# Kernel tuning notes

Measured on AMD Instinct MI355X. Metric: run time of the kernel, lower is better.

Reference implementation:

```python
import jax, jax.numpy as jnp
import numpy as np

D_MODEL = 1024
N_HEADS = 16
HEAD_DIM = D_MODEL // N_HEADS  # 64
BATCH, SEQ = 2, 2048
MASK_FILL = -1000000000.0


def setup_inputs() -> dict:
    key = jax.random.key(0)
    ks = jax.random.split(key, 13)
    s = 1.0 / np.sqrt(D_MODEL)
    inp = {
        "q": jax.random.normal(ks[0], (BATCH, SEQ, D_MODEL), jnp.float32),
        "k": jax.random.normal(ks[1], (BATCH, SEQ, D_MODEL), jnp.float32),
        "v": jax.random.normal(ks[2], (BATCH, SEQ, D_MODEL), jnp.float32),
        "mask": jax.random.randint(ks[3], (BATCH, 1, SEQ, SEQ), 0, 2, jnp.int32),
        "Wq": jax.random.normal(ks[4], (D_MODEL, D_MODEL), jnp.float32) * s,
        "bq": jax.random.normal(ks[5], (D_MODEL,), jnp.float32) * s,
        "Wk": jax.random.normal(ks[6], (D_MODEL, D_MODEL), jnp.float32) * s,
        "bk": jax.random.normal(ks[7], (D_MODEL,), jnp.float32) * s,
        "Wv": jax.random.normal(ks[8], (D_MODEL, D_MODEL), jnp.float32) * s,
        "bv": jax.random.normal(ks[9], (D_MODEL,), jnp.float32) * s,
        "Wo": jax.random.normal(ks[10], (D_MODEL, D_MODEL), jnp.float32) * s,
        "bo": jax.random.normal(ks[11], (D_MODEL,), jnp.float32) * s,
    }
    return inp


def reference(q, k, v, mask, Wq, bq, Wk, bk, Wv, bv, Wo, bo):
    batch, seq, feat = q.shape
    # Linear projections (torch Linear: x @ W.T + b)
    qp = q @ Wq.T + bq
    kp = k @ Wk.T + bk
    vp = v @ Wv.T + bv

    def split(x):
        # (B, S, D) -> (B, H, S, Dh)
        return x.reshape(batch, seq, N_HEADS, HEAD_DIM).swapaxes(1, 2)

    qh, kh, vh = split(qp), split(kp), split(vp)

    # (B, H, S, S) score matrix, scaled
    score = jnp.einsum("bhqd,bhkd->bhqk", qh, kh) / jnp.sqrt(
        jnp.asarray(HEAD_DIM, qh.dtype))
    score = jnp.where(mask == 0, jnp.asarray(MASK_FILL, score.dtype), score)
    attn = jax.nn.softmax(score, axis=-1)
    out = jnp.einsum("bhqk,bhkd->bhqd", attn, vh)  # (B, H, S, Dh)
    joint = out.swapaxes(1, 2).reshape(batch, seq, feat)
    return joint @ Wo.T + bo
```

## Files before the change

### kernel.cpp

```cpp
#include <hip/hip_runtime.h>

typedef unsigned short u16;
typedef unsigned int u32;
typedef unsigned long long u64;
typedef float f32x4 __attribute__((ext_vector_type(4)));
typedef float f32x16 __attribute__((ext_vector_type(16)));
typedef __bf16 bf16x4 __attribute__((ext_vector_type(4)));
typedef __bf16 bf16x8 __attribute__((ext_vector_type(8)));
typedef u16 u16x8 __attribute__((ext_vector_type(8)));
typedef u32 u32x4 __attribute__((ext_vector_type(4)));

#define QSCALE 0.18033688011112042f

__device__ __forceinline__ u16 f2bf(float f) {
  unsigned int u = __float_as_uint(f);
  u += 0x7fffu + ((u >> 16) & 1u);
  return (u16)(u >> 16);
}

__device__ __forceinline__ void async16(const void* g, void* l) {
  __builtin_amdgcn_global_load_lds(
      (__attribute__((address_space(1))) void*)g,
      (__attribute__((address_space(3))) void*)l,
      16, 0, 0);
}

__device__ __forceinline__ f32x4 mfma16(bf16x8 a, bf16x8 b, f32x4 c) {
  return __builtin_amdgcn_mfma_f32_16x16x32_bf16(a, b, c, 0, 0, 0);
}

__device__ __forceinline__ f32x16 mfma32(bf16x8 a, bf16x8 b, f32x16 c) {
  return __builtin_amdgcn_mfma_f32_32x32x16_bf16(a, b, c, 0, 0, 0);
}

__device__ __forceinline__ u32 cvtpk(float lo, float hi) {
  u32 r;
  asm("v_cvt_pk_bf16_f32 %0, %1, %2" : "=v"(r) : "v"(lo), "v"(hi));
  return r;
}

__device__ __forceinline__ void pswap(u32& a, u32& b) {
  asm("v_permlane32_swap_b32 %0, %1" : "+v"(a), "+v"(b));
}

struct CvtArgs {
  const float* src[7];
  u16* dst[7];
};

__global__ __launch_bounds__(256) void cvt_kernel(CvtArgs a) {
  int z = blockIdx.z;
  int n = (z < 3) ? 4194304 : 1048576;
  int base = (blockIdx.x * 256 + threadIdx.x) * 8;
  if (base >= n) return;
  const float* s = a.src[z] + base;
  f32x4 x0 = *(const f32x4*)s;
  f32x4 x1 = *(const f32x4*)(s + 4);
  u16x8 pk;
  pk[0]=f2bf(x0[0]); pk[1]=f2bf(x0[1]); pk[2]=f2bf(x0[2]); pk[3]=f2bf(x0[3]);
  pk[4]=f2bf(x1[0]); pk[5]=f2bf(x1[1]); pk[6]=f2bf(x1[2]); pk[7]=f2bf(x1[3]);
  *(u16x8*)(a.dst[z] + base) = pk;
}

__global__ __launch_bounds__(256) void pack_mask_kernel(
    const int* __restrict__ mask, u64* __restrict__ pm) {
  int idx = blockIdx.x * 256 + threadIdx.x;
  const int4* src = (const int4*)(mask + (size_t)idx * 64);
  u64 bits = 0ull;
#pragma unroll
  for (int j = 0; j < 16; ++j) {
    int4 v = src[j];
    if (v.x) bits |= 1ull << (4 * j + 0);
    if (v.y) bits |= 1ull << (4 * j + 1);
    if (v.z) bits |= 1ull << (4 * j + 2);
    if (v.w) bits |= 1ull << (4 * j + 3);
  }
  pm[idx] = bits;
}

__device__ __forceinline__ void gemm_body(const u16* __restrict__ A,
                                          const u16* __restrict__ W,
                                          const float* __restrict__ bias,
                                          void* __restrict__ outraw, int mode,
                                          float oscale) {
  alignas(16) __shared__ u16 lA[128 * 32];
  alignas(16) __shared__ u16 lB[128 * 32];
  const int tid = threadIdx.x;
  const int lane = tid & 63, wv = tid >> 6;
  const int wm = wv >> 1, wn = wv & 1;
  const int m0 = blockIdx.y * 128, n0 = blockIdx.x * 128;
  const int l15 = lane & 15, quad = lane >> 4;
  const int srow = lane >> 2;
  const int scol = (lane & 3) * 8;

  f32x4 acc[4][4] = {};

  for (int k0 = 0; k0 < 1024; k0 += 32) {
#pragma unroll
    for (int t = 0; t < 2; ++t) {
      int rb = (wv * 2 + t) * 16;
      async16(A + (size_t)(m0 + rb + srow) * 1024 + k0 + scol, (char*)lA + rb * 64);
      async16(W + (size_t)(n0 + rb + srow) * 1024 + k0 + scol, (char*)lB + rb * 64);
    }
    __syncthreads();
    bf16x8 af[4], bfr[4];
#pragma unroll
    for (int i = 0; i < 4; ++i) {
      af[i]  = *(const bf16x8*)(lA + (wm * 64 + i * 16 + l15) * 32 + quad * 8);
      bfr[i] = *(const bf16x8*)(lB + (wn * 64 + i * 16 + l15) * 32 + quad * 8);
    }
#pragma unroll
    for (int i = 0; i < 4; ++i)
#pragma unroll
      for (int j = 0; j < 4; ++j)
        acc[i][j] = mfma16(af[i], bfr[j], acc[i][j]);
    __syncthreads();
  }

#pragma unroll
  for (int i = 0; i < 4; ++i) {
    int mbase = m0 + wm * 64 + i * 16 + quad * 4;
#pragma unroll
    for (int j = 0; j < 4; ++j) {
      int n = n0 + wn * 64 + j * 16 + l15;
      float bv = bias[n];
#pragma unroll
      for (int r = 0; r < 4; ++r) {
        int m = mbase + r;
        float val = (acc[i][j][r] + bv) * oscale;
        if (mode == 0) {
          int b = m >> 11, s = m & 2047, h = n >> 6, dh = n & 63;
          ((u16*)outraw)[((((size_t)b * 16 + h) * 2048 + s) << 6) + dh] = f2bf(val);
        } else if (mode == 1) {
          int b = m >> 11, s = m & 2047, h = n >> 6, dh = n & 63;
          ((u16*)outraw)[((((size_t)b * 16 + h) * 64 + dh) << 11) + s] = f2bf(val);
        } else {
          ((float*)outraw)[(size_t)m * 1024 + n] = val;
        }
      }
    }
  }
}

__global__ __launch_bounds__(256) void gemm_qkv_kernel(
    const u16* __restrict__ qb, const u16* __restrict__ kb, const u16* __restrict__ vb,
    const u16* __restrict__ Wqb, const float* __restrict__ bq,
    const u16* __restrict__ Wkb, const float* __restrict__ bk,
    const u16* __restrict__ Wvb, const float* __restrict__ bv,
    u16* __restrict__ qp, u16* __restrict__ kp, u16* __restrict__ vt) {
  if (blockIdx.z == 0)      gemm_body(qb, Wqb, bq, qp, 0, QSCALE);
  else if (blockIdx.z == 1) gemm_body(kb, Wkb, bk, kp, 0, 1.0f);
  else                      gemm_body(vb, Wvb, bv, vt, 1, 1.0f);
}

__global__ __launch_bounds__(256) void gemm_o_kernel(
    const u16* __restrict__ joint, const u16* __restrict__ Wob,
    const float* __restrict__ bo, float* __restrict__ out) {
  gemm_body(joint, Wob, bo, out, 2, 1.0f);
}

__global__ __launch_bounds__(256, 2) void attn_kernel(
    const u16* __restrict__ qp, const u16* __restrict__ kp,
    const u16* __restrict__ vt, const u64* __restrict__ pm,
    u16* __restrict__ joint) {
  alignas(16) __shared__ u16 kbuf[2][4096];
  alignas(16) __shared__ u16 vbuf[2][4096];

  const int tid = threadIdx.x, lane = tid & 63, wv = tid >> 6;
  const int l31 = lane & 31, hi = lane >> 5, l7 = lane & 7;
  const int q0 = blockIdx.x * 128;
  const int hd = blockIdx.y, b = blockIdx.z;
  const size_t head_off = ((size_t)b * 16 + hd) * 2048 * 64;
  const u16* Qh = qp + head_off;
  const u16* Kh = kp + head_off;
  const u16* Vh = vt + head_off;
  const int qr = q0 + wv * 32 + l31;
  const u64* pmq = pm + ((size_t)b * 2048 + qr) * 32;

  bf16x8 qf[4];
  {
    const u16* qrow = Qh + (size_t)qr * 64 + hi * 8;
#pragma unroll
    for (int d = 0; d < 4; ++d) qf[d] = *(const bf16x8*)(qrow + d * 16);
  }

  const int sd0 = tid, sd1 = 256 + tid;
  const int kr0 = sd0 >> 3, ks0 = ((sd0 & 7) ^ (kr0 & 7)) * 8;
  const int kr1 = sd1 >> 3, ks1 = ((sd1 & 7) ^ (kr1 & 7)) * 8;
  const u16* kg0 = Kh + (size_t)kr0 * 64 + ks0;
  const u16* kg1 = Kh + (size_t)kr1 * 64 + ks1;
  const u16* vg0 = Vh + (size_t)kr0 * 2048 + ks0;
  const u16* vg1 = Vh + (size_t)kr1 * 2048 + ks1;

  f32x16 O[2] = {};
  f32x4 lacc = {};
  const f32x16 fz16 = {};

  async16(kg0, (char*)kbuf[0] + sd0 * 16);
  async16(kg1, (char*)kbuf[0] + sd1 * 16);
  async16(vg0, (char*)vbuf[0] + sd0 * 16);
  async16(vg1, (char*)vbuf[0] + sd1 * 16);

  for (int kt = 0; kt < 32; ++kt) {
    __syncthreads();

    if (kt != 31) {
      const size_t kadv = (size_t)(kt + 1) * 4096;
      const int vadv = (kt + 1) * 64;
      char* kd = (char*)kbuf[(kt + 1) & 1];
      char* vd = (char*)vbuf[(kt + 1) & 1];
      async16(kg0 + kadv, kd + sd0 * 16);
      async16(kg1 + kadv, kd + sd1 * 16);
      async16(vg0 + vadv, vd + sd0 * 16);
      async16(vg1 + vadv, vd + sd1 * 16);
    }

    u64 word = pmq[kt];
    const char* kc = (const char*)kbuf[kt & 1];
    const char* vc = (const char*)vbuf[kt & 1];

    bf16x8 kf[2][4];
#pragma unroll
    for (int h = 0; h < 2; ++h)
#pragma unroll
      for (int d = 0; d < 4; ++d)
        kf[h][d] = *(const bf16x8*)(kc + (h * 32 + l31) * 128 +
                                    (((2 * d + hi) ^ l7) << 4));

    f32x16 S[2];
#pragma unroll
    for (int h = 0; h < 2; ++h) {
      f32x16 s = mfma32(kf[h][0], qf[0], fz16);
      s = mfma32(kf[h][1], qf[1], s);
      s = mfma32(kf[h][2], qf[2], s);
      S[h] = mfma32(kf[h][3], qf[3], s);
    }

    bf16x8 vf[2][4];
#pragma unroll
    for (int g = 0; g < 2; ++g)
#pragma unroll
      for (int ks = 0; ks < 4; ++ks)
        vf[g][ks] = *(const bf16x8*)(vc + (g * 32 + l31) * 128 +
                                     (((2 * ks + hi) ^ l7) << 4));

    {
      const int hi4 = hi * 4;
#pragma unroll
      for (int h = 0; h < 2; ++h) {
        u32 wh = (h == 0) ? (u32)word : (u32)(word >> 32);
#pragma unroll
        for (int rq = 0; rq < 4; ++rq) {
          u32 nib = wh >> (rq * 8 + hi4);
#pragma unroll
          for (int r4 = 0; r4 < 4; ++r4) {
            int i = rq * 4 + r4;
            float pe = __builtin_amdgcn_exp2f(S[h][i]);
            S[h][i] = ((nib >> r4) & 1u) ? pe : 0.f;
          }
          f32x4 sv = {S[h][rq * 4 + 0], S[h][rq * 4 + 1],
                      S[h][rq * 4 + 2], S[h][rq * 4 + 3]};
          lacc += sv;
        }
      }
    }

    bf16x8 pf[4];
#pragma unroll
    for (int ks = 0; ks < 4; ++ks) {
      int h = ks >> 1;
      int ra = (ks & 1) * 8;
      u32 w0a = cvtpk(S[h][ra + 0], S[h][ra + 1]);
      u32 w1a = cvtpk(S[h][ra + 2], S[h][ra + 3]);
      u32 w0b = cvtpk(S[h][ra + 4], S[h][ra + 5]);
      u32 w1b = cvtpk(S[h][ra + 6], S[h][ra + 7]);
      pswap(w0a, w0b);
      pswap(w1a, w1b);
      u32x4 t = {w0a, w1a, w0b, w1b};
      pf[ks] = __builtin_bit_cast(bf16x8, t);
    }

#pragma unroll
    for (int g = 0; g < 2; ++g) {
      f32x16 o = O[g];
      o = mfma32(vf[g][0], pf[0], o);
      o = mfma32(vf[g][1], pf[1], o);
      o = mfma32(vf[g][2], pf[2], o);
      O[g] = mfma32(vf[g][3], pf[3], o);
    }
  }

  {
    float l = (lacc[0] + lacc[1]) + (lacc[2] + lacc[3]);
    l += __shfl_xor(l, 32, 64);
    float inv = 1.0f / l;
    size_t row_off = ((size_t)b * 2048 + qr) * 1024 + hd * 64;
#pragma unroll
    for (int g = 0; g < 2; ++g)
#pragma unroll
      for (int rq = 0; rq < 4; ++rq) {
        f32x4 ov = {O[g][rq * 4 + 0] * inv, O[g][rq * 4 + 1] * inv,
                    O[g][rq * 4 + 2] * inv, O[g][rq * 4 + 3] * inv};
        bf16x4 obv = __builtin_convertvector(ov, bf16x4);
        *(u64*)(joint + row_off + g * 32 + rq * 8 + hi * 4) =
            *(const u64*)&obv;
      }
  }
}

extern "C" void kernel_launch(void* const* d_in, const int* in_sizes, int n_in,
                              void* d_out, int out_size, void* d_ws, size_t ws_size,
                              hipStream_t stream) {
  const float* q  = (const float*)d_in[0];
  const float* k  = (const float*)d_in[1];
  const float* v  = (const float*)d_in[2];
  const int* mask = (const int*)d_in[3];
  const float* Wq = (const float*)d_in[4];
  const float* bq = (const float*)d_in[5];
  const float* Wk = (const float*)d_in[6];
  const float* bk = (const float*)d_in[7];
  const float* Wv = (const float*)d_in[8];
  const float* bv = (const float*)d_in[9];
  const float* Wo = (const float*)d_in[10];
  const float* bo = (const float*)d_in[11];
  float* out = (float*)d_out;

  u16* w = (u16*)d_ws;
  u16* qp    = w;
  u16* kp    = w + 4194304;
  u16* vt    = w + 8388608;
  u16* qb    = w + 12582912;
  u16* kb    = w + 16777216;
  u16* vb    = w + 20971520;
  u16* Wqb   = w + 25165824;
  u16* Wkb   = w + 26214400;
  u16* Wvb   = w + 27262976;
  u16* Wob   = w + 28311552;
  u64* pm    = (u64*)(w + 29360128);
  u16* joint = qb;

  CvtArgs ca;
  ca.src[0] = q;  ca.dst[0] = qb;
  ca.src[1] = k;  ca.dst[1] = kb;
  ca.src[2] = v;  ca.dst[2] = vb;
  ca.src[3] = Wq; ca.dst[3] = Wqb;
  ca.src[4] = Wk; ca.dst[4] = Wkb;
  ca.src[5] = Wv; ca.dst[5] = Wvb;
  ca.src[6] = Wo; ca.dst[6] = Wob;

  pack_mask_kernel<<<dim3(512), dim3(256), 0, stream>>>(mask, pm);
  cvt_kernel<<<dim3(2048, 1, 7), dim3(256), 0, stream>>>(ca);
  gemm_qkv_kernel<<<dim3(8, 32, 3), dim3(256), 0, stream>>>(
      qb, kb, vb, Wqb, bq, Wkb, bk, Wvb, bv, qp, kp, vt);
  attn_kernel<<<dim3(16, 16, 2), dim3(256), 0, stream>>>(qp, kp, vt, pm, joint);
  gemm_o_kernel<<<dim3(8, 32, 1), dim3(256), 0, stream>>>(joint, Wob, bo, out);
}
```

Baseline: 286.1 us.

## Split attention KV tiles across wave pairs and remap grid for XCD locality

Result: faster. 272.2 us (-4.9%).

```diff
diff --git a/kernel.cpp b/kernel.cpp
--- a/kernel.cpp
+++ b/kernel.cpp
@@ -159,23 +159,28 @@
   gemm_body(joint, Wob, bo, out, 2, 1.0f);
 }
 
-__global__ __launch_bounds__(256, 2) void attn_kernel(
+__global__ __launch_bounds__(256, 4) void attn_kernel(
     const u16* __restrict__ qp, const u16* __restrict__ kp,
     const u16* __restrict__ vt, const u64* __restrict__ pm,
     u16* __restrict__ joint) {
-  alignas(16) __shared__ u16 kbuf[2][4096];
-  alignas(16) __shared__ u16 vbuf[2][4096];
+  alignas(16) __shared__ char smem[32768];
 
   const int tid = threadIdx.x, lane = tid & 63, wv = tid >> 6;
   const int l31 = lane & 31, hi = lane >> 5, l7 = lane & 7;
-  const int q0 = blockIdx.x * 128;
-  const int hd = blockIdx.y, b = blockIdx.z;
+  const int qg = wv >> 1, kh = wv & 1;
+
+  const int linear = blockIdx.x;
+  const int xcd = linear & 7, slot = linear >> 3;
+  const int grp = (xcd << 2) | (slot >> 5);
+  const int q0 = (slot & 31) * 64;
+  const int hd = grp & 15, b = grp >> 4;
+
   const size_t head_off = ((size_t)b * 16 + hd) * 2048 * 64;
   const u16* Qh = qp + head_off;
   const u16* Kh = kp + head_off;
   const u16* Vh = vt + head_off;
-  const int qr = q0 + wv * 32 + l31;
-  const u64* pmq = pm + ((size_t)b * 2048 + qr) * 32;
+  const int qr = q0 + qg * 32 + l31;
+  const u32* pmq32 = (const u32*)(pm + ((size_t)b * 2048 + qr) * 32) + kh;
 
   bf16x8 qf[4];
   {
@@ -196,10 +201,10 @@
   f32x4 lacc = {};
   const f32x16 fz16 = {};
 
-  async16(kg0, (char*)kbuf[0] + sd0 * 16);
-  async16(kg1, (char*)kbuf[0] + sd1 * 16);
-  async16(vg0, (char*)vbuf[0] + sd0 * 16);
-  async16(vg1, (char*)vbuf[0] + sd1 * 16);
+  async16(kg0, smem + sd0 * 16);
+  async16(kg1, smem + sd1 * 16);
+  async16(vg0, smem + 16384 + sd0 * 16);
+  async16(vg1, smem + 16384 + sd1 * 16);
 
   for (int kt = 0; kt < 32; ++kt) {
     __syncthreads();
@@ -207,93 +212,101 @@
     if (kt != 31) {
       const size_t kadv = (size_t)(kt + 1) * 4096;
       const int vadv = (kt + 1) * 64;
-      char* kd = (char*)kbuf[(kt + 1) & 1];
-      char* vd = (char*)vbuf[(kt + 1) & 1];
+      char* kd = smem + (((kt + 1) & 1) << 13);
+      char* vd = smem + 16384 + (((kt + 1) & 1) << 13);
       async16(kg0 + kadv, kd + sd0 * 16);
       async16(kg1 + kadv, kd + sd1 * 16);
       async16(vg0 + vadv, vd + sd0 * 16);
       async16(vg1 + vadv, vd + sd1 * 16);
     }
 
-    u64 word = pmq[kt];
-    const char* kc = (const char*)kbuf[kt & 1];
-    const char* vc = (const char*)vbuf[kt & 1];
-
-    bf16x8 kf[2][4];
-#pragma unroll
-    for (int h = 0; h < 2; ++h)
-#pragma unroll
-      for (int d = 0; d < 4; ++d)
-        kf[h][d] = *(const bf16x8*)(kc + (h * 32 + l31) * 128 +
-                                    (((2 * d + hi) ^ l7) << 4));
-
-    f32x16 S[2];
-#pragma unroll
-    for (int h = 0; h < 2; ++h) {
-      f32x16 s = mfma32(kf[h][0], qf[0], fz16);
-      s = mfma32(kf[h][1], qf[1], s);
-      s = mfma32(kf[h][2], qf[2], s);
-      S[h] = mfma32(kf[h][3], qf[3], s);
-    }
-
-    bf16x8 vf[2][4];
+    u32 wh = pmq32[2 * kt];
+    const char* kc = smem + ((kt & 1) << 13);
+    const char* vc = smem + 16384 + ((kt & 1) << 13);
+
+    bf16x8 kf[4];
+#pragma unroll
+    for (int d = 0; d < 4; ++d)
+      kf[d] = *(const bf16x8*)(kc + (kh * 32 + l31) * 128 +
+                               (((2 * d + hi) ^ l7) << 4));
+
+    f32x16 S;
+    {
+      f32x16 s = mfma32(kf[0], qf[0], fz16);
+      s = mfma32(kf[1], qf[1], s);
+      s = mfma32(kf[2], qf[2], s);
+      S = mfma32(kf[3], qf[3], s);
+    }
+
+    bf16x8 vf[2][2];
 #pragma unroll
     for (int g = 0; g < 2; ++g)
 #pragma unroll
-      for (int ks = 0; ks < 4; ++ks)
-        vf[g][ks] = *(const bf16x8*)(vc + (g * 32 + l31) * 128 +
-                                     (((2 * ks + hi) ^ l7) << 4));
+      for (int t = 0; t < 2; ++t) {
+        int ks = kh * 2 + t;
+        vf[g][t] = *(const bf16x8*)(vc + (g * 32 + l31) * 128 +
+                                    (((2 * ks + hi) ^ l7) << 4));
+      }
 
     {
       const int hi4 = hi * 4;
 #pragma unroll
-      for (int h = 0; h < 2; ++h) {
-        u32 wh = (h == 0) ? (u32)word : (u32)(word >> 32);
-#pragma unroll
-        for (int rq = 0; rq < 4; ++rq) {
-          u32 nib = wh >> (rq * 8 + hi4);
-#pragma unroll
-          for (int r4 = 0; r4 < 4; ++r4) {
-            int i = rq * 4 + r4;
-            float pe = __builtin_amdgcn_exp2f(S[h][i]);
-            S[h][i] = ((nib >> r4) & 1u) ? pe : 0.f;
-          }
-          f32x4 sv = {S[h][rq * 4 + 0], S[h][rq * 4 + 1],
-                      S[h][rq * 4 + 2], S[h][rq * 4 + 3]};
-          lacc += sv;
+      for (int rq = 0; rq < 4; ++rq) {
+        u32 nib = wh >> (rq * 8 + hi4);
+#pragma unroll
+        for (int r4 = 0; r4 < 4; ++r4) {
+          int i = rq * 4 + r4;
+          float pe = __builtin_amdgcn_exp2f(S[i]);
+          S[i] = ((nib >> r4) & 1u) ? pe : 0.f;
         }
+        f32x4 sv = {S[rq * 4 + 0], S[rq * 4 + 1], S[rq * 4 + 2], S[rq * 4 + 3]};
+        lacc += sv;
       }
     }
 
-    bf16x8 pf[4];
-#pragma unroll
-    for (int ks = 0; ks < 4; ++ks) {
-      int h = ks >> 1;
-      int ra = (ks & 1) * 8;
-      u32 w0a = cvtpk(S[h][ra + 0], S[h][ra + 1]);
-      u32 w1a = cvtpk(S[h][ra + 2], S[h][ra + 3]);
-      u32 w0b = cvtpk(S[h][ra + 4], S[h][ra + 5]);
-      u32 w1b = cvtpk(S[h][ra + 6], S[h][ra + 7]);
+    bf16x8 pf[2];
+#pragma unroll
+    for (int t = 0; t < 2; ++t) {
+      int ra = t * 8;
+      u32 w0a = cvtpk(S[ra + 0], S[ra + 1]);
+      u32 w1a = cvtpk(S[ra + 2], S[ra + 3]);
+      u32 w0b = cvtpk(S[ra + 4], S[ra + 5]);
+      u32 w1b = cvtpk(S[ra + 6], S[ra + 7]);
       pswap(w0a, w0b);
       pswap(w1a, w1b);
-      u32x4 t = {w0a, w1a, w0b, w1b};
-      pf[ks] = __builtin_bit_cast(bf16x8, t);
+      u32x4 tt = {w0a, w1a, w0b, w1b};
+      pf[t] = __builtin_bit_cast(bf16x8, tt);
     }
 
 #pragma unroll
     for (int g = 0; g < 2; ++g) {
       f32x16 o = O[g];
       o = mfma32(vf[g][0], pf[0], o);
-      o = mfma32(vf[g][1], pf[1], o);
-      o = mfma32(vf[g][2], pf[2], o);
-      O[g] = mfma32(vf[g][3], pf[3], o);
-    }
-  }
-
-  {
-    float l = (lacc[0] + lacc[1]) + (lacc[2] + lacc[3]);
-    l += __shfl_xor(l, 32, 64);
-    float inv = 1.0f / l;
+      O[g] = mfma32(vf[g][1], pf[1], o);
+    }
+  }
+
+  float lp = (lacc[0] + lacc[1]) + (lacc[2] + lacc[3]);
+  lp += __shfl_xor(lp, 32, 64);
+  __syncthreads();
+  float* exch = (float*)smem;
+  if (kh == 1) {
+    float* e = exch + (qg * 64 + lane) * 34;
+#pragma unroll
+    for (int g = 0; g < 2; ++g)
+#pragma unroll
+      for (int i = 0; i < 16; ++i) e[g * 16 + i] = O[g][i];
+    e[32] = lp;
+  }
+  __syncthreads();
+  if (kh == 0) {
+    const float* e = exch + (qg * 64 + lane) * 34;
+#pragma unroll
+    for (int g = 0; g < 2; ++g)
+#pragma unroll
+      for (int i = 0; i < 16; ++i) O[g][i] += e[g * 16 + i];
+    lp += e[32];
+    float inv = 1.0f / lp;
     size_t row_off = ((size_t)b * 2048 + qr) * 1024 + hd * 64;
 #pragma unroll
     for (int g = 0; g < 2; ++g)
@@ -352,6 +365,6 @@
   cvt_kernel<<<dim3(2048, 1, 7), dim3(256), 0, stream>>>(ca);
   gemm_qkv_kernel<<<dim3(8, 32, 3), dim3(256), 0, stream>>>(
       qb, kb, vb, Wqb, bq, Wkb, bk, Wvb, bv, qp, kp, vt);
-  attn_kernel<<<dim3(16, 16, 2), dim3(256), 0, stream>>>(qp, kp, vt, pm, joint);
+  attn_kernel<<<dim3(1024), dim3(256), 0, stream>>>(qp, kp, vt, pm, joint);
   gemm_o_kernel<<<dim3(8, 32, 1), dim3(256), 0, stream>>>(joint, Wob, bo, out);
 }
```
